# Optimization experiments

Hardware: AMD Instinct MI355X
Metric: run time of the kernel (lower is better)

The kernel has to match this reference:

```python
import jax, jax.numpy as jnp
import numpy as np

D_MODEL = 1024
NUM_HEADS = 16
HEAD_DIM = D_MODEL // NUM_HEADS


def setup_inputs() -> dict:
    key = jax.random.key(0)
    ks = jax.random.split(key, 9)
    B, S = 4, 2048
    bound = 1.0 / np.sqrt(D_MODEL)  # nn.Linear default init range
    def lin(kw, kb):
        W = jax.random.uniform(kw, (D_MODEL, D_MODEL), jnp.float32, -bound, bound)
        b = jax.random.uniform(kb, (D_MODEL,), jnp.float32, -bound, bound)
        return W, b
    Wq, bq = lin(ks[0], ks[1])
    Wk, bk = lin(ks[2], ks[3])
    Wv, bv = lin(ks[4], ks[5])
    Wo, bo = lin(ks[6], ks[7])
    x = jax.random.normal(ks[8], (B, S, D_MODEL), jnp.float32)
    return {"x": x, "Wq": Wq, "bq": bq, "Wk": Wk, "bk": bk,
            "Wv": Wv, "bv": bv, "Wo": Wo, "bo": bo}


def reference(x, Wq, bq, Wk, bk, Wv, bv, Wo, bo):
    B, S, _ = x.shape
    scale = 1.0 / np.sqrt(HEAD_DIM)
    # projections; torch Linear is x @ W.T + b; here W stored as [in, out]-style [d,d] already transposed
    def split_heads(t):
        return t.reshape(B, S, NUM_HEADS, HEAD_DIM).transpose(0, 2, 1, 3)  # [B,H,S,Dh]
    q = split_heads(x @ Wq + bq)
    k = split_heads(x @ Wk + bk)
    v = split_heads(x @ Wv + bv)
    scores = jnp.einsum('bhqd,bhkd->bhqk', q, k) * scale  # [B,H,S,S]
    attn = jax.nn.softmax(scores, axis=-1)
    out = jnp.einsum('bhqk,bhkd->bhqd', attn, v)  # [B,H,S,Dh]
    out = out.transpose(0, 2, 1, 3).reshape(B, S, D_MODEL)
    return out @ Wo + bo
```

## Files before the change

### kernel.cpp

```cpp
#include <hip/hip_runtime.h>
#include <hip/hip_bf16.h>

typedef __attribute__((ext_vector_type(8))) short short8;
typedef __attribute__((ext_vector_type(4))) float f32x4;
typedef __attribute__((ext_vector_type(16))) float f32x16;

#define MFMA16(a, b, c) __builtin_amdgcn_mfma_f32_16x16x32_bf16((a), (b), (c), 0, 0, 0)
#define MFMA32(a, b, c) __builtin_amdgcn_mfma_f32_32x32x16_bf16((a), (b), (c), 0, 0, 0)

__device__ __forceinline__ void gload_lds16(const void* g, void* l) {
  __builtin_amdgcn_global_load_lds(
      (const __attribute__((address_space(1))) unsigned int*)g,
      (__attribute__((address_space(3))) unsigned int*)l, 16, 0, 0);
}

__global__ __launch_bounds__(256) void cvt_x(const float* __restrict__ x,
                                             __hip_bfloat16* __restrict__ xb) {
  size_t i = ((size_t)blockIdx.x * 256 + threadIdx.x) * 8;
  float4 a = *(const float4*)(x + i);
  float4 b = *(const float4*)(x + i + 4);
  struct alignas(16) B8 { __hip_bfloat16 h[8]; } o;
  o.h[0] = __float2bfloat16(a.x); o.h[1] = __float2bfloat16(a.y);
  o.h[2] = __float2bfloat16(a.z); o.h[3] = __float2bfloat16(a.w);
  o.h[4] = __float2bfloat16(b.x); o.h[5] = __float2bfloat16(b.y);
  o.h[6] = __float2bfloat16(b.z); o.h[7] = __float2bfloat16(b.w);
  *(B8*)(xb + i) = o;
}

__global__ __launch_bounds__(256) void trans_w(const float* __restrict__ W0,
                                               const float* __restrict__ W1,
                                               const float* __restrict__ W2,
                                               const float* __restrict__ W3,
                                               __hip_bfloat16* __restrict__ Wt) {
  const int which = blockIdx.z;
  const float* W = (which == 0) ? W0 : (which == 1) ? W1 : (which == 2) ? W2 : W3;
  __hip_bfloat16* O = Wt + (size_t)which * 1024 * 1024;
  __shared__ __hip_bfloat16 lds[64][65];
  const int k0 = blockIdx.y * 64, n0 = blockIdx.x * 64;
#pragma unroll
  for (int i = 0; i < 16; ++i) {
    int idx = threadIdx.x + i * 256;
    int r = idx >> 6, c = idx & 63;
    lds[r][c] = __float2bfloat16(W[(size_t)(k0 + r) * 1024 + n0 + c]);
  }
  __syncthreads();
#pragma unroll
  for (int i = 0; i < 16; ++i) {
    int idx = threadIdx.x + i * 256;
    int r = idx >> 6, c = idx & 63;
    O[(size_t)(n0 + r) * 1024 + k0 + c] = lds[c][r];
  }
}

template <int MODE>
__global__ __launch_bounds__(256) void gemm_bt(const __hip_bfloat16* __restrict__ A,
                                               const __hip_bfloat16* __restrict__ Bt,
                                               const float* __restrict__ bias,
                                               void* __restrict__ outp, int M) {
  const int N = 1024, K = 1024;
  __shared__ __hip_bfloat16 Asm[128 * 32];
  __shared__ __hip_bfloat16 Bsm[128 * 32];
  const int t = threadIdx.x;
  const int lane = t & 63, w = t >> 6, g = lane >> 4;
  const int nbn = N / 128;
  const int mb0 = (blockIdx.x / nbn) * 128;
  const int nb0 = (blockIdx.x % nbn) * 128;
  const int wr = (w >> 1) * 64, wc = (w & 1) * 64;
  f32x4 acc[4][4] = {};

  for (int k0 = 0; k0 < K; k0 += 32) {
    __syncthreads();
#pragma unroll
    for (int i = 0; i < 2; ++i) {
      int tp = i * 256 + t;
      int row = tp >> 2;
      int slot = (tp & 3) ^ ((row >> 1) & 3);
      gload_lds16(A + (size_t)(mb0 + row) * K + k0 + slot * 8,
                  (char*)Asm + (i * 256 + w * 64) * 16);
    }
#pragma unroll
    for (int i = 0; i < 2; ++i) {
      int tp = i * 256 + t;
      int row = tp >> 2;
      int slot = (tp & 3) ^ ((row >> 1) & 3);
      gload_lds16(Bt + (size_t)(nb0 + row) * K + k0 + slot * 8,
                  (char*)Bsm + (i * 256 + w * 64) * 16);
    }
    asm volatile("s_waitcnt vmcnt(0)" ::: "memory");
    __syncthreads();

    short8 a[4], b[4];
#pragma unroll
    for (int m = 0; m < 4; ++m) {
      int row = wr + m * 16 + (lane & 15);
      a[m] = *(const short8*)((const char*)Asm + row * 64 + ((g ^ ((row >> 1) & 3)) * 16));
    }
#pragma unroll
    for (int n = 0; n < 4; ++n) {
      int row = wc + n * 16 + (lane & 15);
      b[n] = *(const short8*)((const char*)Bsm + row * 64 + ((g ^ ((row >> 1) & 3)) * 16));
    }
#pragma unroll
    for (int m = 0; m < 4; ++m)
#pragma unroll
      for (int n = 0; n < 4; ++n)
        acc[m][n] = MFMA16(a[m], b[n], acc[m][n]);
  }

#pragma unroll
  for (int n = 0; n < 4; ++n) {
    int col = nb0 + wc + n * 16 + (lane & 15);
    float bv = bias[col];
#pragma unroll
    for (int m = 0; m < 4; ++m) {
#pragma unroll
      for (int r = 0; r < 4; ++r) {
        int row = mb0 + wr + m * 16 + g * 4 + r;
        float v = acc[m][n][r] + bv;
        if (MODE == 0) {
          ((__hip_bfloat16*)outp)[(size_t)row * N + col] = __float2bfloat16(v);
        } else if (MODE == 1) {
          int bb = row >> 11, s = row & 2047;
          int sp = (s & ~12) | ((s & 4) << 1) | ((s & 8) >> 1);
          ((__hip_bfloat16*)outp)[((size_t)(bb * 1024 + col) << 11) + sp] = __float2bfloat16(v);
        } else {
          ((float*)outp)[(size_t)row * N + col] = v;
        }
      }
    }
  }
}

__global__ __launch_bounds__(256, 4) void attn_fwd3(const __hip_bfloat16* __restrict__ Q,
                                                    const __hip_bfloat16* __restrict__ Kg,
                                                    const __hip_bfloat16* __restrict__ Vt,
                                                    __hip_bfloat16* __restrict__ ctx) {
  __shared__ __hip_bfloat16 Ksm[2][64 * 64];
  __shared__ __hip_bfloat16 Vsm[2][64 * 64];
  const int t = threadIdx.x, lane = t & 63, w = t >> 6;
  const int l31 = lane & 31, hi = lane >> 5;
  const int bid = (blockIdx.x & 7) * 128 + (blockIdx.x >> 3);
  const int bh = bid >> 4, qt = bid & 15;
  const int b = bh >> 4, h = bh & 15;
  const int q = qt * 128 + w * 32 + l31;

  short8 qf[4];
  {
    const __hip_bfloat16* qp = Q + ((size_t)(b * 2048 + q)) * 1024 + h * 64 + hi * 8;
#pragma unroll
    for (int c = 0; c < 4; ++c) qf[c] = *(const short8*)(qp + 16 * c);
  }
  const __hip_bfloat16* Kbh = Kg + (size_t)b * 2048 * 1024 + h * 64;
  const __hip_bfloat16* Vbh = Vt + (size_t)(b * 16 + h) * 64 * 2048;

  const int srow = t >> 3;
  const int sslot = t & 7;

#define STAGE(buf, ktn)                                                          \
  do {                                                                           \
    _Pragma("unroll") for (int i = 0; i < 2; ++i) {                              \
      int row = i * 32 + srow;                                                   \
      int sl = sslot ^ (row & 7);                                                \
      gload_lds16(Kbh + (size_t)((ktn) + row) * 1024 + sl * 8,                   \
                  (char*)&Ksm[buf][0] + i * 4096 + w * 1024);                    \
      gload_lds16(Vbh + (size_t)row * 2048 + (ktn) + sl * 8,                     \
                  (char*)&Vsm[buf][0] + i * 4096 + w * 1024);                    \
    }                                                                            \
  } while (0)

  f32x16 ot0 = {}, ot1 = {};
  float ls0 = 0.f, ls1 = 0.f, ls2 = 0.f, ls3 = 0.f;
  const float CL = 0.18033688011112042f;
  const float NEG = -43.28085122666891f;

  STAGE(0, 0);
  asm volatile("s_waitcnt vmcnt(0)" ::: "memory");
  __syncthreads();

  for (int kt = 0; kt < 2048; kt += 64) {
    const int cur = (kt >> 6) & 1;
    if (kt + 64 < 2048) STAGE(cur ^ 1, kt + 64);

    const char* Kb0 = (const char*)&Ksm[cur][0];
    const char* Vb0 = (const char*)&Vsm[cur][0];
    short8 kf[2][4], vf[2][4];
#pragma unroll
    for (int s = 0; s < 2; ++s)
#pragma unroll
      for (int c = 0; c < 4; ++c) {
        int row = s * 32 + l31;
        kf[s][c] = *(const short8*)(Kb0 + row * 128 + (((hi + 2 * c) ^ (row & 7)) * 16));
      }
#pragma unroll
    for (int dt = 0; dt < 2; ++dt)
#pragma unroll
      for (int c = 0; c < 4; ++c) {
        int row = dt * 32 + l31;
        vf[dt][c] = *(const short8*)(Vb0 + row * 128 + (((hi + 2 * c) ^ (row & 7)) * 16));
      }

    f32x16 st0 = {}, st1 = {};
#pragma unroll
    for (int c = 0; c < 4; ++c) st0 = MFMA32(kf[0][c], qf[c], st0);
#pragma unroll
    for (int c = 0; c < 4; ++c) st1 = MFMA32(kf[1][c], qf[c], st1);

    float p[32];
#pragma unroll
    for (int j = 0; j < 16; ++j) {
      float arg = __builtin_fmaf(st0[j], CL, NEG);
      asm("v_exp_f32 %0, %1" : "=v"(p[j]) : "v"(arg));
    }
#pragma unroll
    for (int j = 0; j < 16; ++j) {
      float arg = __builtin_fmaf(st1[j], CL, NEG);
      asm("v_exp_f32 %0, %1" : "=v"(p[16 + j]) : "v"(arg));
    }
#pragma unroll
    for (int j = 0; j < 32; j += 4) {
      ls0 += p[j]; ls1 += p[j + 1]; ls2 += p[j + 2]; ls3 += p[j + 3];
    }

    unsigned q32[16];
#pragma unroll
    for (int n = 0; n < 16; ++n)
      asm("v_cvt_pk_bf16_f32 %0, %1, %2" : "=v"(q32[n]) : "v"(p[2 * n]), "v"(p[2 * n + 1]));

#pragma unroll
    for (int c = 0; c < 4; ++c) {
      union { unsigned u[4]; short8 s8; } pb;
      pb.u[0] = q32[4 * c]; pb.u[1] = q32[4 * c + 1];
      pb.u[2] = q32[4 * c + 2]; pb.u[3] = q32[4 * c + 3];
      ot0 = MFMA32(vf[0][c], pb.s8, ot0);
      ot1 = MFMA32(vf[1][c], pb.s8, ot1);
    }

    asm volatile("s_waitcnt vmcnt(0)" ::: "memory");
    __syncthreads();
  }
#undef STAGE

  float lsum = ls0 + ls1 + ls2 + ls3;
  lsum += __shfl_xor(lsum, 32);
  float inv = 1.0f / lsum;

  __hip_bfloat16* op = ctx + ((size_t)(b * 2048 + q)) * 1024 + h * 64 + 4 * hi;
#pragma unroll
  for (int dt = 0; dt < 2; ++dt) {
#pragma unroll
    for (int g = 0; g < 4; ++g) {
      struct alignas(8) H4 { __hip_bfloat16 x[4]; } o4;
#pragma unroll
      for (int e = 0; e < 4; ++e)
        o4.x[e] = __float2bfloat16((dt ? ot1[4 * g + e] : ot0[4 * g + e]) * inv);
      *(H4*)(op + 32 * dt + 8 * g) = o4;
    }
  }
}

extern "C" void kernel_launch(void* const* d_in, const int* in_sizes, int n_in,
                              void* d_out, int out_size, void* d_ws, size_t ws_size,
                              hipStream_t stream) {
  (void)in_sizes; (void)n_in; (void)out_size; (void)ws_size;
  const float* x  = (const float*)d_in[0];
  const float* Wq = (const float*)d_in[1];
  const float* bq = (const float*)d_in[2];
  const float* Wk = (const float*)d_in[3];
  const float* bk = (const float*)d_in[4];
  const float* Wv = (const float*)d_in[5];
  const float* bv = (const float*)d_in[6];
  const float* Wo = (const float*)d_in[7];
  const float* bo = (const float*)d_in[8];
  float* out = (float*)d_out;

  __hip_bfloat16* ws  = (__hip_bfloat16*)d_ws;
  __hip_bfloat16* xb  = ws;
  __hip_bfloat16* Wt  = xb + 8388608;
  __hip_bfloat16* Qb  = Wt + 4194304;
  __hip_bfloat16* Kb  = Qb + 8388608;
  __hip_bfloat16* Vtb = Kb + 8388608;
  __hip_bfloat16* ctx = xb;

  cvt_x<<<4096, 256, 0, stream>>>(x, xb);
  trans_w<<<dim3(16, 16, 4), 256, 0, stream>>>(Wq, Wk, Wv, Wo, Wt);
  gemm_bt<0><<<64 * 8, 256, 0, stream>>>(xb, Wt,           bq, Qb,  8192);
  gemm_bt<0><<<64 * 8, 256, 0, stream>>>(xb, Wt + 1048576, bk, Kb,  8192);
  gemm_bt<1><<<64 * 8, 256, 0, stream>>>(xb, Wt + 2097152, bv, Vtb, 8192);
  attn_fwd3<<<1024, 256, 0, stream>>>(Qb, Kb, Vtb, ctx);
  gemm_bt<2><<<64 * 8, 256, 0, stream>>>(ctx, Wt + 3145728, bo, out, 8192);
}
```

Measured before the change: 224.1 us.

## Fuse QKV GEMMs into one launch, swizzle block order, add setprio and unrolled attention loop

After: 369.0 us. +64.6%, slower.

```diff
diff --git a/kernel.cpp b/kernel.cpp
--- a/kernel.cpp
+++ b/kernel.cpp
@@ -52,19 +52,26 @@
   }
 }
 
-template <int MODE>
-__global__ __launch_bounds__(256) void gemm_bt(const __hip_bfloat16* __restrict__ A,
-                                               const __hip_bfloat16* __restrict__ Bt,
-                                               const float* __restrict__ bias,
-                                               void* __restrict__ outp, int M) {
-  const int N = 1024, K = 1024;
+__global__ __launch_bounds__(256) void gemm_qkv(const __hip_bfloat16* __restrict__ A,
+                                                const __hip_bfloat16* __restrict__ Wt,
+                                                const float* __restrict__ bq,
+                                                const float* __restrict__ bk,
+                                                const float* __restrict__ bv,
+                                                __hip_bfloat16* __restrict__ Qb,
+                                                __hip_bfloat16* __restrict__ Kb,
+                                                __hip_bfloat16* __restrict__ Vtb) {
+  const int K = 1024;
   __shared__ __hip_bfloat16 Asm[128 * 32];
   __shared__ __hip_bfloat16 Bsm[128 * 32];
   const int t = threadIdx.x;
   const int lane = t & 63, w = t >> 6, g = lane >> 4;
-  const int nbn = N / 128;
-  const int mb0 = (blockIdx.x / nbn) * 128;
-  const int nb0 = (blockIdx.x % nbn) * 128;
+  const int bid = (blockIdx.x & 7) * 192 + (blockIdx.x >> 3);
+  const int mb0 = (bid / 24) * 128;
+  const int nbg = (bid % 24) * 128;
+  const int which = nbg >> 10;
+  const int nb0 = nbg & 1023;
+  const __hip_bfloat16* Bt = Wt + (size_t)which * 1048576;
+  const float* bias = (which == 0) ? bq : (which == 1) ? bk : bv;
   const int wr = (w >> 1) * 64, wc = (w & 1) * 64;
   f32x4 acc[4][4] = {};
 
@@ -110,28 +117,89 @@
 #pragma unroll
   for (int n = 0; n < 4; ++n) {
     int col = nb0 + wc + n * 16 + (lane & 15);
-    float bv = bias[col];
+    float bvv = bias[col];
 #pragma unroll
     for (int m = 0; m < 4; ++m) {
 #pragma unroll
       for (int r = 0; r < 4; ++r) {
         int row = mb0 + wr + m * 16 + g * 4 + r;
-        float v = acc[m][n][r] + bv;
-        if (MODE == 0) {
-          ((__hip_bfloat16*)outp)[(size_t)row * N + col] = __float2bfloat16(v);
-        } else if (MODE == 1) {
+        __hip_bfloat16 hv = __float2bfloat16(acc[m][n][r] + bvv);
+        if (which == 2) {
           int bb = row >> 11, s = row & 2047;
           int sp = (s & ~12) | ((s & 4) << 1) | ((s & 8) >> 1);
-          ((__hip_bfloat16*)outp)[((size_t)(bb * 1024 + col) << 11) + sp] = __float2bfloat16(v);
+          Vtb[((size_t)(bb * 1024 + col) << 11) + sp] = hv;
         } else {
-          ((float*)outp)[(size_t)row * N + col] = v;
+          __hip_bfloat16* O = which ? Kb : Qb;
+          O[(size_t)row * 1024 + col] = hv;
         }
       }
     }
   }
 }
 
-__global__ __launch_bounds__(256, 4) void attn_fwd3(const __hip_bfloat16* __restrict__ Q,
+__global__ __launch_bounds__(256) void gemm_o(const __hip_bfloat16* __restrict__ A,
+                                              const __hip_bfloat16* __restrict__ Bt,
+                                              const float* __restrict__ bias,
+                                              float* __restrict__ outp) {
+  const int N = 1024, K = 1024;
+  __shared__ __hip_bfloat16 Asm[128 * 32];
+  __shared__ __hip_bfloat16 Bsm[128 * 32];
+  const int t = threadIdx.x;
+  const int lane = t & 63, w = t >> 6, g = lane >> 4;
+  const int bid = (blockIdx.x & 7) * 64 + (blockIdx.x >> 3);
+  const int mb0 = (bid / 8) * 128;
+  const int nb0 = (bid % 8) * 128;
+  const int wr = (w >> 1) * 64, wc = (w & 1) * 64;
+  f32x4 acc[4][4] = {};
+
+  for (int k0 = 0; k0 < K; k0 += 32) {
+    __syncthreads();
+#pragma unroll
+    for (int i = 0; i < 2; ++i) {
+      int tp = i * 256 + t;
+      int row = tp >> 2;
+      int slot = (tp & 3) ^ ((row >> 1) & 3);
+      gload_lds16(A + (size_t)(mb0 + row) * K + k0 + slot * 8,
+                  (char*)Asm + (i * 256 + w * 64) * 16);
+      gload_lds16(Bt + (size_t)(nb0 + row) * K + k0 + slot * 8,
+                  (char*)Bsm + (i * 256 + w * 64) * 16);
+    }
+    asm volatile("s_waitcnt vmcnt(0)" ::: "memory");
+    __syncthreads();
+
+    short8 a[4], b[4];
+#pragma unroll
+    for (int m = 0; m < 4; ++m) {
+      int row = wr + m * 16 + (lane & 15);
+      a[m] = *(const short8*)((const char*)Asm + row * 64 + ((g ^ ((row >> 1) & 3)) * 16));
+    }
+#pragma unroll
+    for (int n = 0; n < 4; ++n) {
+      int row = wc + n * 16 + (lane & 15);
+      b[n] = *(const short8*)((const char*)Bsm + row * 64 + ((g ^ ((row >> 1) & 3)) * 16));
+    }
+#pragma unroll
+    for (int m = 0; m < 4; ++m)
+#pragma unroll
+      for (int n = 0; n < 4; ++n)
+        acc[m][n] = MFMA16(a[m], b[n], acc[m][n]);
+  }
+
+#pragma unroll
+  for (int n = 0; n < 4; ++n) {
+    int col = nb0 + wc + n * 16 + (lane & 15);
+    float bvv = bias[col];
+#pragma unroll
+    for (int m = 0; m < 4; ++m)
+#pragma unroll
+      for (int r = 0; r < 4; ++r) {
+        int row = mb0 + wr + m * 16 + g * 4 + r;
+        outp[(size_t)row * N + col] = acc[m][n][r] + bvv;
+      }
+  }
+}
+
+__global__ __launch_bounds__(256, 4) void attn_fwd4(const __hip_bfloat16* __restrict__ Q,
                                                     const __hip_bfloat16* __restrict__ Kg,
                                                     const __hip_bfloat16* __restrict__ Vt,
                                                     __hip_bfloat16* __restrict__ ctx) {
@@ -173,72 +241,72 @@
   const float CL = 0.18033688011112042f;
   const float NEG = -43.28085122666891f;
 
+#define BODY(buf)                                                                 \
+  do {                                                                            \
+    const char* Kb0 = (const char*)&Ksm[buf][0];                                  \
+    const char* Vb0 = (const char*)&Vsm[buf][0];                                  \
+    short8 kf[2][4], vf[2][4];                                                    \
+    _Pragma("unroll") for (int s = 0; s < 2; ++s)                                 \
+      _Pragma("unroll") for (int c = 0; c < 4; ++c) {                             \
+        int row = s * 32 + l31;                                                   \
+        kf[s][c] = *(const short8*)(Kb0 + row * 128 + (((hi + 2 * c) ^ (row & 7)) * 16)); \
+      }                                                                           \
+    _Pragma("unroll") for (int dt = 0; dt < 2; ++dt)                              \
+      _Pragma("unroll") for (int c = 0; c < 4; ++c) {                             \
+        int row = dt * 32 + l31;                                                  \
+        vf[dt][c] = *(const short8*)(Vb0 + row * 128 + (((hi + 2 * c) ^ (row & 7)) * 16)); \
+      }                                                                           \
+    f32x16 st0 = {}, st1 = {};                                                    \
+    __builtin_amdgcn_s_setprio(1);                                                \
+    _Pragma("unroll") for (int c = 0; c < 4; ++c) st0 = MFMA32(kf[0][c], qf[c], st0); \
+    _Pragma("unroll") for (int c = 0; c < 4; ++c) st1 = MFMA32(kf[1][c], qf[c], st1); \
+    __builtin_amdgcn_s_setprio(0);                                                \
+    float p[32];                                                                  \
+    _Pragma("unroll") for (int j = 0; j < 16; ++j) {                              \
+      float arg = __builtin_fmaf(st0[j], CL, NEG);                                \
+      asm("v_exp_f32 %0, %1" : "=v"(p[j]) : "v"(arg));                            \
+    }                                                                             \
+    _Pragma("unroll") for (int j = 0; j < 16; ++j) {                              \
+      float arg = __builtin_fmaf(st1[j], CL, NEG);                                \
+      asm("v_exp_f32 %0, %1" : "=v"(p[16 + j]) : "v"(arg));                       \
+    }                                                                             \
+    _Pragma("unroll") for (int j = 0; j < 32; j += 4) {                           \
+      ls0 += p[j]; ls1 += p[j + 1]; ls2 += p[j + 2]; ls3 += p[j + 3];             \
+    }                                                                             \
+    unsigned q32[16];                                                             \
+    _Pragma("unroll") for (int n = 0; n < 16; ++n)                                \
+      asm("v_cvt_pk_bf16_f32 %0, %1, %2" : "=v"(q32[n]) : "v"(p[2 * n]), "v"(p[2 * n + 1])); \
+    __builtin_amdgcn_s_setprio(1);                                                \
+    _Pragma("unroll") for (int c = 0; c < 4; ++c) {                               \
+      union { unsigned u[4]; short8 s8; } pb;                                     \
+      pb.u[0] = q32[4 * c]; pb.u[1] = q32[4 * c + 1];                             \
+      pb.u[2] = q32[4 * c + 2]; pb.u[3] = q32[4 * c + 3];                         \
+      ot0 = MFMA32(vf[0][c], pb.s8, ot0);                                         \
+      ot1 = MFMA32(vf[1][c], pb.s8, ot1);                                         \
+    }                                                                             \
+    __builtin_amdgcn_s_setprio(0);                                                \
+  } while (0)
+
+#define DRAIN()                                          \
+  do {                                                   \
+    asm volatile("s_waitcnt vmcnt(0)" ::: "memory");     \
+    __syncthreads();                                     \
+  } while (0)
+
   STAGE(0, 0);
-  asm volatile("s_waitcnt vmcnt(0)" ::: "memory");
-  __syncthreads();
-
-  for (int kt = 0; kt < 2048; kt += 64) {
-    const int cur = (kt >> 6) & 1;
-    if (kt + 64 < 2048) STAGE(cur ^ 1, kt + 64);
-
-    const char* Kb0 = (const char*)&Ksm[cur][0];
-    const char* Vb0 = (const char*)&Vsm[cur][0];
-    short8 kf[2][4], vf[2][4];
-#pragma unroll
-    for (int s = 0; s < 2; ++s)
-#pragma unroll
-      for (int c = 0; c < 4; ++c) {
-        int row = s * 32 + l31;
-        kf[s][c] = *(const short8*)(Kb0 + row * 128 + (((hi + 2 * c) ^ (row & 7)) * 16));
-      }
-#pragma unroll
-    for (int dt = 0; dt < 2; ++dt)
-#pragma unroll
-      for (int c = 0; c < 4; ++c) {
-        int row = dt * 32 + l31;
-        vf[dt][c] = *(const short8*)(Vb0 + row * 128 + (((hi + 2 * c) ^ (row & 7)) * 16));
-      }
-
-    f32x16 st0 = {}, st1 = {};
-#pragma unroll
-    for (int c = 0; c < 4; ++c) st0 = MFMA32(kf[0][c], qf[c], st0);
-#pragma unroll
-    for (int c = 0; c < 4; ++c) st1 = MFMA32(kf[1][c], qf[c], st1);
-
-    float p[32];
-#pragma unroll
-    for (int j = 0; j < 16; ++j) {
-      float arg = __builtin_fmaf(st0[j], CL, NEG);
-      asm("v_exp_f32 %0, %1" : "=v"(p[j]) : "v"(arg));
-    }
-#pragma unroll
-    for (int j = 0; j < 16; ++j) {
-      float arg = __builtin_fmaf(st1[j], CL, NEG);
-      asm("v_exp_f32 %0, %1" : "=v"(p[16 + j]) : "v"(arg));
-    }
-#pragma unroll
-    for (int j = 0; j < 32; j += 4) {
-      ls0 += p[j]; ls1 += p[j + 1]; ls2 += p[j + 2]; ls3 += p[j + 3];
-    }
-
-    unsigned q32[16];
-#pragma unroll
-    for (int n = 0; n < 16; ++n)
-      asm("v_cvt_pk_bf16_f32 %0, %1, %2" : "=v"(q32[n]) : "v"(p[2 * n]), "v"(p[2 * n + 1]));
-
-#pragma unroll
-    for (int c = 0; c < 4; ++c) {
-      union { unsigned u[4]; short8 s8; } pb;
-      pb.u[0] = q32[4 * c]; pb.u[1] = q32[4 * c + 1];
-      pb.u[2] = q32[4 * c + 2]; pb.u[3] = q32[4 * c + 3];
-      ot0 = MFMA32(vf[0][c], pb.s8, ot0);
-      ot1 = MFMA32(vf[1][c], pb.s8, ot1);
-    }
-
-    asm volatile("s_waitcnt vmcnt(0)" ::: "memory");
-    __syncthreads();
+  DRAIN();
+
+  for (int kt = 0; kt < 2048; kt += 128) {
+    STAGE(1, kt + 64);
+    BODY(0);
+    DRAIN();
+    if (kt + 128 < 2048) STAGE(0, kt + 128);
+    BODY(1);
+    DRAIN();
   }
 #undef STAGE
+#undef BODY
+#undef DRAIN
 
   float lsum = ls0 + ls1 + ls2 + ls3;
   lsum += __shfl_xor(lsum, 32);
@@ -283,9 +351,7 @@
 
   cvt_x<<<4096, 256, 0, stream>>>(x, xb);
   trans_w<<<dim3(16, 16, 4), 256, 0, stream>>>(Wq, Wk, Wv, Wo, Wt);
-  gemm_bt<0><<<64 * 8, 256, 0, stream>>>(xb, Wt,           bq, Qb,  8192);
-  gemm_bt<0><<<64 * 8, 256, 0, stream>>>(xb, Wt + 1048576, bk, Kb,  8192);
-  gemm_bt<1><<<64 * 8, 256, 0, stream>>>(xb, Wt + 2097152, bv, Vtb, 8192);
-  attn_fwd3<<<1024, 256, 0, stream>>>(Qb, Kb, Vtb, ctx);
-  gemm_bt<2><<<64 * 8, 256, 0, stream>>>(ctx, Wt + 3145728, bo, out, 8192);
-}
+  gemm_qkv<<<1536, 256, 0, stream>>>(xb, Wt, bq, bk, bv, Qb, Kb, Vtb);
+  attn_fwd4<<<1024, 256, 0, stream>>>(Qb, Kb, Vtb, ctx);
+  gemm_o<<<512, 256, 0, stream>>>(ctx, Wt + 3145728, bo, out);
+}
```
